# Performance work log

Hardware: AMD Instinct MI355X
Metric: run time of the kernel (lower is better)

## Reference

```python
import jax, jax.numpy as jnp
import numpy as np

N_NODES = 100000
N_EDGES = 800000
N_FEAT = 64
H_DIM = 64
N_GRAPHS = 64


def _glorot(key, fan_in, fan_out):
    lim = np.sqrt(6.0 / (fan_in + fan_out)).astype(np.float32)
    return jax.random.uniform(key, (fan_in, fan_out), jnp.float32, -lim, lim)


def setup_inputs() -> dict:
    key = jax.random.key(0)
    ks = jax.random.split(key, 10)
    x = jax.random.normal(ks[0], (N_NODES, N_FEAT), jnp.float32)
    edge_index = jax.random.randint(ks[1], (2, N_EDGES), 0, N_NODES, dtype=jnp.int64)
    batch = jnp.sort(jax.random.randint(ks[2], (N_NODES,), 0, N_GRAPHS, dtype=jnp.int64))
    return {
        "x": x,
        "edge_index": edge_index,
        "batch": batch,
        "W0": _glorot(ks[3], N_FEAT, H_DIM), "b0": jnp.zeros((H_DIM,), jnp.float32),
        "W1": _glorot(ks[4], H_DIM, H_DIM), "b1": jnp.zeros((H_DIM,), jnp.float32),
        "W2": _glorot(ks[5], H_DIM, H_DIM), "b2": jnp.zeros((H_DIM,), jnp.float32),
        "Wl": _glorot(ks[6], H_DIM, H_DIM),
        "bl": jax.random.normal(ks[7], (H_DIM,), jnp.float32) * 0.01,
    }


def _gcn_conv(h, W, b, row, col, dinv_r, dinv_c, n_nodes):
    # PyG GCNConv: x W, then sym-normalized aggregation over edges+self-loops
    h = h @ W                                   # [N, H]
    msg = h[row] * (dinv_r * dinv_c)[:, None]   # gather + scale, [E+N, H]
    out = jax.ops.segment_sum(msg, col, num_segments=n_nodes)  # scatter-add
    return out + b


def reference(x, edge_index, batch, W0, b0, W1, b1, W2, b2, Wl, bl):
    n = x.shape[0]
    loops = jnp.arange(n, dtype=edge_index.dtype)
    row = jnp.concatenate([edge_index[0], loops])  # source nodes (+self-loops)
    col = jnp.concatenate([edge_index[1], loops])  # destination nodes
    deg = jax.ops.segment_sum(jnp.ones_like(col, dtype=x.dtype), col, num_segments=n)
    dinv = jnp.where(deg > 0, jax.lax.rsqrt(deg), 0.0)
    dinv_r, dinv_c = dinv[row], dinv[col]

    out = x
    for W, b in ((W0, b0), (W1, b1), (W2, b2)):
        out = jax.nn.relu(_gcn_conv(out, W, b, row, col, dinv_r, dinv_c, n))
        # F.dropout(training=False) is identity in eval mode
    return (out, out @ Wl + bl)
```

## Files before the change

kernel.cpp:

```cpp
#include <hip/hip_runtime.h>

#define NN 100000
#define NE 800000
#define HD 64
#define BK 128
#define NBUCK ((NN + BK - 1) / BK)
#define PA_EPT 16
#define PA_NB ((NE + 256 * PA_EPT - 1) / (256 * PA_EPT))
#define LDW 68
#define LDB 72

typedef __attribute__((ext_vector_type(8))) short bf16x8;
typedef __attribute__((ext_vector_type(4))) float f32x4;

__device__ __forceinline__ int load_idx(const void* ei, int i, bool is32) {
    if (is32) return ((const int*)ei)[i];
    return (int)(((const long long*)ei)[i]);
}

__device__ __forceinline__ unsigned short f2bf(float f) {
    unsigned u = __float_as_uint(f);
    return (unsigned short)((u + 0x7FFFu + ((u >> 16) & 1u)) >> 16);
}

__device__ __forceinline__ float bf2f(unsigned short h) {
    return __uint_as_float((unsigned)h << 16);
}

__device__ __forceinline__ void bfacc(const uint4& u, float4& a, float4& b) {
    a.x += __uint_as_float(u.x << 16);
    a.y += __uint_as_float(u.x & 0xFFFF0000u);
    a.z += __uint_as_float(u.y << 16);
    a.w += __uint_as_float(u.y & 0xFFFF0000u);
    b.x += __uint_as_float(u.z << 16);
    b.y += __uint_as_float(u.z & 0xFFFF0000u);
    b.z += __uint_as_float(u.w << 16);
    b.w += __uint_as_float(u.w & 0xFFFF0000u);
}

__global__ void k_initdet(const void* ei, int* bcnt, int* flag) {
    __shared__ int bad;
    int t = threadIdx.x;
    if (t == 0) bad = 0;
    if (t < NBUCK) bcnt[t] = 0;
    __syncthreads();
    const long long* p = (const long long*)ei;
    for (int i = t; i < 4096; i += 1024) {
        long long v = p[i];
        if (v < 0 || v >= (long long)NN) bad = 1;
    }
    __syncthreads();
    if (t == 0) *flag = bad ? 1 : 0;
}

__global__ __launch_bounds__(256) void k_pass0(const void* ei, const int* flag,
                                               int* bcnt) {
    __shared__ int h[NBUCK];
    for (int i = threadIdx.x; i < NBUCK; i += 256) h[i] = 0;
    __syncthreads();
    bool is32 = (*flag != 0);
    int stride = gridDim.x * 256;
    for (int e = blockIdx.x * 256 + threadIdx.x; e < NE; e += stride) {
        int dst = load_idx(ei, NE + e, is32);
        atomicAdd(&h[dst >> 7], 1);
    }
    __syncthreads();
    for (int i = threadIdx.x; i < NBUCK; i += 256) {
        int v = h[i];
        if (v) atomicAdd(&bcnt[i], v);
    }
}

__global__ __launch_bounds__(256) void k_scan1(const int* __restrict__ bcnt,
                                               int* __restrict__ offs,
                                               int* __restrict__ curs) {
    __shared__ int sc[256];
    int t = threadIdx.x;
    int v[4], s = 0;
#pragma unroll
    for (int i = 0; i < 4; ++i) {
        int b = t * 4 + i;
        v[i] = (b < NBUCK) ? bcnt[b] : 0;
        s += v[i];
    }
    sc[t] = s;
    __syncthreads();
    for (int off = 1; off < 256; off <<= 1) {
        int add = (t >= off) ? sc[t - off] : 0;
        __syncthreads();
        sc[t] += add;
        __syncthreads();
    }
    int run = sc[t] - s;
#pragma unroll
    for (int i = 0; i < 4; ++i) {
        int b = t * 4 + i;
        if (b < NBUCK) { offs[b] = run; curs[b] = run; }
        run += v[i];
    }
    if (t == 255) offs[NBUCK] = sc[255];
}

__global__ __launch_bounds__(256) void k_passA(const void* ei, const int* flag,
                                               int* curs, unsigned* ebuf) {
    __shared__ int h[NBUCK];
    __shared__ int base[NBUCK];
    for (int i = threadIdx.x; i < NBUCK; i += 256) h[i] = 0;
    __syncthreads();
    bool is32 = (*flag != 0);
    int e0 = blockIdx.x * (256 * PA_EPT);
    int src[PA_EPT], dst[PA_EPT];
#pragma unroll
    for (int i = 0; i < PA_EPT; ++i) {
        int e = e0 + i * 256 + threadIdx.x;
        if (e < NE) {
            src[i] = load_idx(ei, e, is32);
            dst[i] = load_idx(ei, NE + e, is32);
            atomicAdd(&h[dst[i] >> 7], 1);
        } else dst[i] = -1;
    }
    __syncthreads();
    for (int i = threadIdx.x; i < NBUCK; i += 256) {
        int v = h[i];
        base[i] = v ? atomicAdd(&curs[i], v) : 0;
        h[i] = 0;
    }
    __syncthreads();
#pragma unroll
    for (int i = 0; i < PA_EPT; ++i) {
        if (dst[i] >= 0) {
            int b = dst[i] >> 7;
            int p = base[b] + atomicAdd(&h[b], 1);
            ebuf[p] = (unsigned)src[i] | ((unsigned)(dst[i] & 127) << 17);
        }
    }
}

__global__ __launch_bounds__(256) void k_passB(const unsigned* __restrict__ ebuf,
                                               const int* __restrict__ offs,
                                               int* __restrict__ noffs,
                                               int* __restrict__ csr_src,
                                               float* __restrict__ dinv) {
    __shared__ int cnt[BK];
    __shared__ int sc[BK];
    __shared__ int nbase[BK];
    __shared__ int rank[BK];
    int bk = blockIdx.x;
    int t = threadIdx.x;
    if (t < BK) { cnt[t] = 0; rank[t] = 0; }
    __syncthreads();
    int rs = offs[bk], re = offs[bk + 1];
    for (int i = rs + t; i < re; i += 256)
        atomicAdd(&cnt[ebuf[i] >> 17], 1);
    __syncthreads();
    if (t < BK) sc[t] = cnt[t];
    __syncthreads();
    for (int off = 1; off < BK; off <<= 1) {
        int v = 0;
        if (t < BK && t >= off) v = sc[t - off];
        __syncthreads();
        if (t < BK) sc[t] += v;
        __syncthreads();
    }
    if (t < BK) {
        int node = bk * BK + t;
        int nb = rs + sc[t] - cnt[t];
        nbase[t] = nb;
        if (node < NN) {
            noffs[node] = nb;
            dinv[node] = rsqrtf((float)(cnt[t] + 1));
        }
    }
    if (bk == NBUCK - 1 && t == 0) noffs[NN] = re;
    __syncthreads();
    for (int i = rs + t; i < re; i += 256) {
        unsigned w = ebuf[i];
        int dl = w >> 17;
        int p = nbase[dl] + atomicAdd(&rank[dl], 1);
        csr_src[p] = (int)(w & 0x1FFFFu);
    }
}

template <bool BIAS, bool PRE, bool BF16OUT>
__global__ __launch_bounds__(256, 4) void k_gemm(const float* __restrict__ X,
                                                 const float* __restrict__ W,
                                                 const float* __restrict__ bias,
                                                 const float* __restrict__ dinv,
                                                 void* __restrict__ Hout, int n) {
    __shared__ float Ws[64 * LDW];
    __shared__ float Xs[128 * LDW];
    int t = threadIdx.x;
    int row0 = blockIdx.x * 128;
    const float4* X4 = (const float4*)X;
    for (int i = t; i < 64 * 16; i += 256) {
        float4 v = ((const float4*)W)[i];
        *(float4*)&Ws[(i >> 4) * LDW + (i & 15) * 4] = v;
    }
    for (int i = t; i < 128 * 16; i += 256) {
        int r = row0 + (i >> 4);
        float4 v = (r < n) ? X4[(size_t)r * 16 + (i & 15)]
                           : make_float4(0.f, 0.f, 0.f, 0.f);
        *(float4*)&Xs[(i >> 4) * LDW + (i & 15) * 4] = v;
    }
    __syncthreads();
    int tc = (t & 15) * 4;
    int rbase = t >> 4;
    float4 acc[8] = {};
#pragma unroll 1
    for (int k = 0; k < 64; k += 4) {
        float4 wv[4], xv[8];
#pragma unroll
        for (int kk = 0; kk < 4; ++kk)
            wv[kk] = *(const float4*)&Ws[(k + kk) * LDW + tc];
#pragma unroll
        for (int i = 0; i < 8; ++i)
            xv[i] = *(const float4*)&Xs[(rbase + 16 * i) * LDW + k];
#pragma unroll
        for (int i = 0; i < 8; ++i) {
            acc[i].x += xv[i].x * wv[0].x + xv[i].y * wv[1].x
                      + xv[i].z * wv[2].x + xv[i].w * wv[3].x;
            acc[i].y += xv[i].x * wv[0].y + xv[i].y * wv[1].y
                      + xv[i].z * wv[2].y + xv[i].w * wv[3].y;
            acc[i].z += xv[i].x * wv[0].z + xv[i].y * wv[1].z
                      + xv[i].z * wv[2].z + xv[i].w * wv[3].z;
            acc[i].w += xv[i].x * wv[0].w + xv[i].y * wv[1].w
                      + xv[i].z * wv[2].w + xv[i].w * wv[3].w;
        }
    }
    float4 bv = make_float4(0.f, 0.f, 0.f, 0.f);
    if (BIAS) bv = *(const float4*)&bias[tc];
#pragma unroll
    for (int i = 0; i < 8; ++i) {
        int r = row0 + rbase + 16 * i;
        if (r < n) {
            float s = PRE ? dinv[r] : 1.f;
            float4 o;
            o.x = (acc[i].x + bv.x) * s;
            o.y = (acc[i].y + bv.y) * s;
            o.z = (acc[i].z + bv.z) * s;
            o.w = (acc[i].w + bv.w) * s;
            if (BF16OUT) {
                ushort4 p;
                p.x = f2bf(o.x); p.y = f2bf(o.y); p.z = f2bf(o.z); p.w = f2bf(o.w);
                ((ushort4*)Hout)[(size_t)r * 16 + (t & 15)] = p;
            } else {
                ((float4*)Hout)[(size_t)r * 16 + (t & 15)] = o;
            }
        }
    }
}

template <int MODE>
__global__ __launch_bounds__(256, 4) void k_fused(const uint4* __restrict__ Hb,
                                               const int* __restrict__ noffs,
                                               const int* __restrict__ csr_src,
                                               const float* __restrict__ dinv,
                                               const float4* __restrict__ b4,
                                               const float* __restrict__ Wn,
                                               const float* __restrict__ bl,
                                               unsigned short* __restrict__ HbOut,
                                               float4* __restrict__ out0,
                                               float* __restrict__ out1) {
    __shared__ unsigned short WtH[64 * LDB];
    __shared__ unsigned short WtL[64 * LDB];
    __shared__ __align__(16) char scratch[32 * LDB * 2 * 2];
    __shared__ float dvs[32];
    __shared__ float bls[64];
    unsigned short* rows_hi = (unsigned short*)scratch;
    unsigned short* rows_lo = (unsigned short*)scratch + 32 * LDB;
    float* cbuf = (float*)scratch;
    int t = threadIdx.x;
    for (int i = t; i < 64 * 64; i += 256) {
        int k = i >> 6, c = i & 63;
        float wv = Wn[i];
        unsigned short hi = f2bf(wv);
        unsigned short lo = f2bf(wv - bf2f(hi));
        WtH[c * LDB + k] = hi;
        WtL[c * LDB + k] = lo;
    }
    if (MODE == 1 && t < 64) bls[t] = bl[t];

    int lane = t & 63;
    int cl = lane >> 3;
    int q = lane & 7;
    int cbase = lane & ~7;
    int nl = (t >> 6) * 8 + cl;
    int base = blockIdx.x * 32;
    int node = base + nl;
    float dv = 0.f;
    float4 alo = make_float4(0.f, 0.f, 0.f, 0.f);
    float4 ahi = make_float4(0.f, 0.f, 0.f, 0.f);
    if (node < NN) {
        dv = dinv[node];
        {
            uint4 u = Hb[(size_t)node * 8 + q];
            bfacc(u, alo, ahi);
        }
        int e0 = noffs[node], e1 = noffs[node + 1];
#pragma unroll 1
        for (int e = e0; e < e1; e += 8) {
            int rem = e1 - e;
            int idx = (q < rem) ? csr_src[e + q] : 0;
            int s[8];
#pragma unroll
            for (int j = 0; j < 8; ++j)
                s[j] = __shfl(idx, cbase + j, 64);
            uint4 uu[8];
#pragma unroll
            for (int j = 0; j < 8; ++j)
                uu[j] = Hb[(size_t)s[j] * 8 + q];
#pragma unroll
            for (int j = 0; j < 8; ++j)
                if (j < rem) bfacc(uu[j], alo, ahi);
        }
    }
    if (node < NN) {
        float4 b0v = b4[2 * q], b1v = b4[2 * q + 1];
        float f[8];
        f[0] = fmaxf(alo.x * dv + b0v.x, 0.f);
        f[1] = fmaxf(alo.y * dv + b0v.y, 0.f);
        f[2] = fmaxf(alo.z * dv + b0v.z, 0.f);
        f[3] = fmaxf(alo.w * dv + b0v.w, 0.f);
        f[4] = fmaxf(ahi.x * dv + b1v.x, 0.f);
        f[5] = fmaxf(ahi.y * dv + b1v.y, 0.f);
        f[6] = fmaxf(ahi.z * dv + b1v.z, 0.f);
        f[7] = fmaxf(ahi.w * dv + b1v.w, 0.f);
        if (MODE == 1) {
            out0[(size_t)node * 16 + 2 * q]     = make_float4(f[0], f[1], f[2], f[3]);
            out0[(size_t)node * 16 + 2 * q + 1] = make_float4(f[4], f[5], f[6], f[7]);
        }
        unsigned hw[4], lw[4];
#pragma unroll
        for (int i = 0; i < 4; ++i) {
            unsigned short h0 = f2bf(f[2 * i]),     h1 = f2bf(f[2 * i + 1]);
            unsigned short l0 = f2bf(f[2 * i]     - bf2f(h0));
            unsigned short l1 = f2bf(f[2 * i + 1] - bf2f(h1));
            hw[i] = (unsigned)h0 | ((unsigned)h1 << 16);
            lw[i] = (unsigned)l0 | ((unsigned)l1 << 16);
        }
        *(uint4*)&rows_hi[nl * LDB + 8 * q] = make_uint4(hw[0], hw[1], hw[2], hw[3]);
        *(uint4*)&rows_lo[nl * LDB + 8 * q] = make_uint4(lw[0], lw[1], lw[2], lw[3]);
        if (q == 0) dvs[nl] = dv;
    }
    __syncthreads();

    int w = t >> 6;
    int la = lane & 15, kc = lane >> 4;
    int tr = w & 1;
    int c0 = (w >> 1) * 32;
    f32x4 ac0 = {0.f, 0.f, 0.f, 0.f};
    f32x4 ac1 = {0.f, 0.f, 0.f, 0.f};
    const unsigned short* arH = &rows_hi[(tr * 16 + la) * LDB];
    const unsigned short* arL = &rows_lo[(tr * 16 + la) * LDB];
    const unsigned short* b0H = &WtH[(c0 + la) * LDB];
    const unsigned short* b0L = &WtL[(c0 + la) * LDB];
    const unsigned short* b1H = &WtH[(c0 + 16 + la) * LDB];
    const unsigned short* b1L = &WtL[(c0 + 16 + la) * LDB];
#pragma unroll
    for (int kh = 0; kh < 2; ++kh) {
        int ko = kh * 32 + kc * 8;
        bf16x8 aH  = *(const bf16x8*)(arH + ko);
        bf16x8 aL  = *(const bf16x8*)(arL + ko);
        bf16x8 bH0 = *(const bf16x8*)(b0H + ko);
        bf16x8 bL0 = *(const bf16x8*)(b0L + ko);
        bf16x8 bH1 = *(const bf16x8*)(b1H + ko);
        bf16x8 bL1 = *(const bf16x8*)(b1L + ko);
        ac0 = __builtin_amdgcn_mfma_f32_16x16x32_bf16(aH, bH0, ac0, 0, 0, 0);
        ac1 = __builtin_amdgcn_mfma_f32_16x16x32_bf16(aH, bH1, ac1, 0, 0, 0);
        ac0 = __builtin_amdgcn_mfma_f32_16x16x32_bf16(aL, bH0, ac0, 0, 0, 0);
        ac1 = __builtin_amdgcn_mfma_f32_16x16x32_bf16(aL, bH1, ac1, 0, 0, 0);
        ac0 = __builtin_amdgcn_mfma_f32_16x16x32_bf16(aH, bL0, ac0, 0, 0, 0);
        ac1 = __builtin_amdgcn_mfma_f32_16x16x32_bf16(aH, bL1, ac1, 0, 0, 0);
    }
    __syncthreads();

    int rb2 = tr * 16 + kc * 4;
#pragma unroll
    for (int j = 0; j < 4; ++j) {
        cbuf[(rb2 + j) * LDW + c0 + la]      = ac0[j];
        cbuf[(rb2 + j) * LDW + c0 + 16 + la] = ac1[j];
    }
    __syncthreads();

    int nl2 = t >> 3, q2 = t & 7;
    int n2 = base + nl2;
    if (n2 < NN) {
        const float* cp = &cbuf[nl2 * LDW + 8 * q2];
        if (MODE == 0) {
            float s = dvs[nl2];
            ushort4 pa, pb;
            pa.x = f2bf(cp[0] * s); pa.y = f2bf(cp[1] * s);
            pa.z = f2bf(cp[2] * s); pa.w = f2bf(cp[3] * s);
            pb.x = f2bf(cp[4] * s); pb.y = f2bf(cp[5] * s);
            pb.z = f2bf(cp[6] * s); pb.w = f2bf(cp[7] * s);
            *(ushort4*)&HbOut[(size_t)n2 * 64 + 8 * q2]     = pa;
            *(ushort4*)&HbOut[(size_t)n2 * 64 + 8 * q2 + 4] = pb;
        } else {
            float4 o0, o1;
            o0.x = cp[0] + bls[8 * q2];     o0.y = cp[1] + bls[8 * q2 + 1];
            o0.z = cp[2] + bls[8 * q2 + 2]; o0.w = cp[3] + bls[8 * q2 + 3];
            o1.x = cp[4] + bls[8 * q2 + 4]; o1.y = cp[5] + bls[8 * q2 + 5];
            o1.z = cp[6] + bls[8 * q2 + 6]; o1.w = cp[7] + bls[8 * q2 + 7];
            *(float4*)&out1[(size_t)n2 * 64 + 8 * q2]     = o0;
            *(float4*)&out1[(size_t)n2 * 64 + 8 * q2 + 4] = o1;
        }
    }
}

extern "C" void kernel_launch(void* const* d_in, const int* in_sizes, int n_in,
                              void* d_out, int out_size, void* d_ws, size_t ws_size,
                              hipStream_t stream) {
    const float* x  = (const float*)d_in[0];
    const void*  ei = d_in[1];
    const float* W0 = (const float*)d_in[3];
    const float* b0 = (const float*)d_in[4];
    const float* W1 = (const float*)d_in[5];
    const float* b1 = (const float*)d_in[6];
    const float* W2 = (const float*)d_in[7];
    const float* b2 = (const float*)d_in[8];
    const float* Wl = (const float*)d_in[9];
    const float* bl = (const float*)d_in[10];

    char* ws = (char*)d_ws;
    int*      flag    = (int*)(ws);
    int*      bcnt    = (int*)(ws + 256);
    int*      offs    = (int*)(ws + 4352);
    int*      curs    = (int*)(ws + 8448);
    float*    dinv    = (float*)(ws + 12544);
    int*      noffs   = (int*)(ws + 412672);
    int*      csr_src = (int*)(ws + 812800);
    unsigned short* HbA = (unsigned short*)(ws + 4100096);
    unsigned short* HbB = (unsigned short*)(ws + 16900096);

    float* out0 = (float*)d_out;
    float* out1 = out0 + (size_t)NN * HD;
    unsigned* ebuf = (unsigned*)out1;

    int gG = (NN + 127) / 128;
    int gF = (NN + 31) / 32;

    k_initdet<<<1, 1024, 0, stream>>>(ei, bcnt, flag);
    k_pass0<<<128, 256, 0, stream>>>(ei, flag, bcnt);
    k_scan1<<<1, 256, 0, stream>>>(bcnt, offs, curs);
    k_passA<<<PA_NB, 256, 0, stream>>>(ei, flag, curs, ebuf);
    k_passB<<<NBUCK, 256, 0, stream>>>(ebuf, offs, noffs, csr_src, dinv);

    k_gemm<false, true, true><<<gG, 256, 0, stream>>>(x, W0, nullptr, dinv,
                                                      (void*)HbA, NN);
    k_fused<0><<<gF, 256, 0, stream>>>((const uint4*)HbA, noffs, csr_src, dinv,
                                       (const float4*)b0, W1, nullptr,
                                       HbB, nullptr, nullptr);
    k_fused<0><<<gF, 256, 0, stream>>>((const uint4*)HbB, noffs, csr_src, dinv,
                                       (const float4*)b1, W2, nullptr,
                                       HbA, nullptr, nullptr);
    k_fused<1><<<gF, 256, 0, stream>>>((const uint4*)HbA, noffs, csr_src, dinv,
                                       (const float4*)b2, Wl, bl,
                                       nullptr, (float4*)out0, out1);
}
```

Before: 235.2 us.

## Store fp32 weights in LDS and split to bf16 hi/lo at MFMA time

The fused aggregate+GEMM kernel now keeps W and the aggregated rows as fp32 in shared memory and does the bf16 hi/lo split on the fly when building MFMA fragments, instead of pre-splitting into two bf16 arrays. This shrinks LDS use per block, and the occupancy hint rises from 4 to 6 blocks per CU. The node's degree, edge offsets and self feature row are now loaded before the weight staging so their latency overlaps it, and the bias is read from global memory instead of LDS. In exchange, every wave repeats the bf16 conversion work for each fragment, and the tighter launch bound may cause register spills.

New measurement: 241.5 us. 2.7% more time.

```diff
diff --git a/kernel.cpp b/kernel.cpp
--- a/kernel.cpp
+++ b/kernel.cpp
@@ -8,7 +8,6 @@
 #define PA_EPT 16
 #define PA_NB ((NE + 256 * PA_EPT - 1) / (256 * PA_EPT))
 #define LDW 68
-#define LDB 72
 
 typedef __attribute__((ext_vector_type(8))) short bf16x8;
 typedef __attribute__((ext_vector_type(4))) float f32x4;
@@ -36,6 +35,18 @@
     b.y += __uint_as_float(u.z & 0xFFFF0000u);
     b.z += __uint_as_float(u.w << 16);
     b.w += __uint_as_float(u.w & 0xFFFF0000u);
+}
+
+__device__ __forceinline__ void mk_frag(const float* p, bf16x8& h, bf16x8& l) {
+    float4 v0 = *(const float4*)(p);
+    float4 v1 = *(const float4*)(p + 4);
+    float f[8] = {v0.x, v0.y, v0.z, v0.w, v1.x, v1.y, v1.z, v1.w};
+#pragma unroll
+    for (int i = 0; i < 8; ++i) {
+        unsigned short hb = f2bf(f[i]);
+        h[i] = (short)hb;
+        l[i] = (short)f2bf(f[i] - bf2f(hb));
+    }
 }
 
 __global__ void k_initdet(const void* ei, int* bcnt, int* flag) {
@@ -251,7 +262,7 @@
 }
 
 template <int MODE>
-__global__ __launch_bounds__(256, 4) void k_fused(const uint4* __restrict__ Hb,
+__global__ __launch_bounds__(256, 6) void k_fused(const uint4* __restrict__ Hb,
                                                const int* __restrict__ noffs,
                                                const int* __restrict__ csr_src,
                                                const float* __restrict__ dinv,
@@ -261,25 +272,10 @@
                                                unsigned short* __restrict__ HbOut,
                                                float4* __restrict__ out0,
                                                float* __restrict__ out1) {
-    __shared__ unsigned short WtH[64 * LDB];
-    __shared__ unsigned short WtL[64 * LDB];
-    __shared__ __align__(16) char scratch[32 * LDB * 2 * 2];
+    __shared__ float WsT[64 * LDW];
+    __shared__ __align__(16) float rowsb[32 * LDW];
     __shared__ float dvs[32];
-    __shared__ float bls[64];
-    unsigned short* rows_hi = (unsigned short*)scratch;
-    unsigned short* rows_lo = (unsigned short*)scratch + 32 * LDB;
-    float* cbuf = (float*)scratch;
     int t = threadIdx.x;
-    for (int i = t; i < 64 * 64; i += 256) {
-        int k = i >> 6, c = i & 63;
-        float wv = Wn[i];
-        unsigned short hi = f2bf(wv);
-        unsigned short lo = f2bf(wv - bf2f(hi));
-        WtH[c * LDB + k] = hi;
-        WtL[c * LDB + k] = lo;
-    }
-    if (MODE == 1 && t < 64) bls[t] = bl[t];
-
     int lane = t & 63;
     int cl = lane >> 3;
     int q = lane & 7;
@@ -287,16 +283,31 @@
     int nl = (t >> 6) * 8 + cl;
     int base = blockIdx.x * 32;
     int node = base + nl;
+
     float dv = 0.f;
+    int e0 = 0, e1 = 0;
+    uint4 uself = make_uint4(0u, 0u, 0u, 0u);
+    if (node < NN) {
+        dv = dinv[node];
+        e0 = noffs[node];
+        e1 = noffs[node + 1];
+        uself = Hb[(size_t)node * 8 + q];
+    }
+
+    for (int i = t; i < 1024; i += 256) {
+        int k = i & 63;
+        int cg = i >> 6;
+        float4 v = ((const float4*)Wn)[k * 16 + cg];
+        WsT[(cg * 4 + 0) * LDW + k] = v.x;
+        WsT[(cg * 4 + 1) * LDW + k] = v.y;
+        WsT[(cg * 4 + 2) * LDW + k] = v.z;
+        WsT[(cg * 4 + 3) * LDW + k] = v.w;
+    }
+
     float4 alo = make_float4(0.f, 0.f, 0.f, 0.f);
     float4 ahi = make_float4(0.f, 0.f, 0.f, 0.f);
     if (node < NN) {
-        dv = dinv[node];
-        {
-            uint4 u = Hb[(size_t)node * 8 + q];
-            bfacc(u, alo, ahi);
-        }
-        int e0 = noffs[node], e1 = noffs[node + 1];
+        bfacc(uself, alo, ahi);
 #pragma unroll 1
         for (int e = e0; e < e1; e += 8) {
             int rem = e1 - e;
@@ -316,30 +327,21 @@
     }
     if (node < NN) {
         float4 b0v = b4[2 * q], b1v = b4[2 * q + 1];
-        float f[8];
-        f[0] = fmaxf(alo.x * dv + b0v.x, 0.f);
-        f[1] = fmaxf(alo.y * dv + b0v.y, 0.f);
-        f[2] = fmaxf(alo.z * dv + b0v.z, 0.f);
-        f[3] = fmaxf(alo.w * dv + b0v.w, 0.f);
-        f[4] = fmaxf(ahi.x * dv + b1v.x, 0.f);
-        f[5] = fmaxf(ahi.y * dv + b1v.y, 0.f);
-        f[6] = fmaxf(ahi.z * dv + b1v.z, 0.f);
-        f[7] = fmaxf(ahi.w * dv + b1v.w, 0.f);
+        float4 r0, r1;
+        r0.x = fmaxf(alo.x * dv + b0v.x, 0.f);
+        r0.y = fmaxf(alo.y * dv + b0v.y, 0.f);
+        r0.z = fmaxf(alo.z * dv + b0v.z, 0.f);
+        r0.w = fmaxf(alo.w * dv + b0v.w, 0.f);
+        r1.x = fmaxf(ahi.x * dv + b1v.x, 0.f);
+        r1.y = fmaxf(ahi.y * dv + b1v.y, 0.f);
+        r1.z = fmaxf(ahi.z * dv + b1v.z, 0.f);
+        r1.w = fmaxf(ahi.w * dv + b1v.w, 0.f);
         if (MODE == 1) {
-            out0[(size_t)node * 16 + 2 * q]     = make_float4(f[0], f[1], f[2], f[3]);
-            out0[(size_t)node * 16 + 2 * q + 1] = make_float4(f[4], f[5], f[6], f[7]);
-        }
-        unsigned hw[4], lw[4];
-#pragma unroll
-        for (int i = 0; i < 4; ++i) {
-            unsigned short h0 = f2bf(f[2 * i]),     h1 = f2bf(f[2 * i + 1]);
-            unsigned short l0 = f2bf(f[2 * i]     - bf2f(h0));
-            unsigned short l1 = f2bf(f[2 * i + 1] - bf2f(h1));
-            hw[i] = (unsigned)h0 | ((unsigned)h1 << 16);
-            lw[i] = (unsigned)l0 | ((unsigned)l1 << 16);
-        }
-        *(uint4*)&rows_hi[nl * LDB + 8 * q] = make_uint4(hw[0], hw[1], hw[2], hw[3]);
-        *(uint4*)&rows_lo[nl * LDB + 8 * q] = make_uint4(lw[0], lw[1], lw[2], lw[3]);
+            out0[(size_t)node * 16 + 2 * q]     = r0;
+            out0[(size_t)node * 16 + 2 * q + 1] = r1;
+        }
+        *(float4*)&rowsb[nl * LDW + 8 * q]     = r0;
+        *(float4*)&rowsb[nl * LDW + 8 * q + 4] = r1;
         if (q == 0) dvs[nl] = dv;
     }
     __syncthreads();
@@ -350,21 +352,16 @@
     int c0 = (w >> 1) * 32;
     f32x4 ac0 = {0.f, 0.f, 0.f, 0.f};
     f32x4 ac1 = {0.f, 0.f, 0.f, 0.f};
-    const unsigned short* arH = &rows_hi[(tr * 16 + la) * LDB];
-    const unsigned short* arL = &rows_lo[(tr * 16 + la) * LDB];
-    const unsigned short* b0H = &WtH[(c0 + la) * LDB];
-    const unsigned short* b0L = &WtL[(c0 + la) * LDB];
-    const unsigned short* b1H = &WtH[(c0 + 16 + la) * LDB];
-    const unsigned short* b1L = &WtL[(c0 + 16 + la) * LDB];
+    const float* ar  = &rowsb[(tr * 16 + la) * LDW];
+    const float* bp0 = &WsT[(c0 + la) * LDW];
+    const float* bp1 = &WsT[(c0 + 16 + la) * LDW];
 #pragma unroll
     for (int kh = 0; kh < 2; ++kh) {
         int ko = kh * 32 + kc * 8;
-        bf16x8 aH  = *(const bf16x8*)(arH + ko);
-        bf16x8 aL  = *(const bf16x8*)(arL + ko);
-        bf16x8 bH0 = *(const bf16x8*)(b0H + ko);
-        bf16x8 bL0 = *(const bf16x8*)(b0L + ko);
-        bf16x8 bH1 = *(const bf16x8*)(b1H + ko);
-        bf16x8 bL1 = *(const bf16x8*)(b1L + ko);
+        bf16x8 aH, aL, bH0, bL0, bH1, bL1;
+        mk_frag(ar + ko, aH, aL);
+        mk_frag(bp0 + ko, bH0, bL0);
+        mk_frag(bp1 + ko, bH1, bL1);
         ac0 = __builtin_amdgcn_mfma_f32_16x16x32_bf16(aH, bH0, ac0, 0, 0, 0);
         ac1 = __builtin_amdgcn_mfma_f32_16x16x32_bf16(aH, bH1, ac1, 0, 0, 0);
         ac0 = __builtin_amdgcn_mfma_f32_16x16x32_bf16(aL, bH0, ac0, 0, 0, 0);
@@ -374,6 +371,7 @@
     }
     __syncthreads();
 
+    float* cbuf = rowsb;
     int rb2 = tr * 16 + kc * 4;
 #pragma unroll
     for (int j = 0; j < 4; ++j) {
@@ -396,11 +394,13 @@
             *(ushort4*)&HbOut[(size_t)n2 * 64 + 8 * q2]     = pa;
             *(ushort4*)&HbOut[(size_t)n2 * 64 + 8 * q2 + 4] = pb;
         } else {
+            const float4* blv = (const float4*)bl;
+            float4 bv0 = blv[2 * q2], bv1 = blv[2 * q2 + 1];
             float4 o0, o1;
-            o0.x = cp[0] + bls[8 * q2];     o0.y = cp[1] + bls[8 * q2 + 1];
-            o0.z = cp[2] + bls[8 * q2 + 2]; o0.w = cp[3] + bls[8 * q2 + 3];
-            o1.x = cp[4] + bls[8 * q2 + 4]; o1.y = cp[5] + bls[8 * q2 + 5];
-            o1.z = cp[6] + bls[8 * q2 + 6]; o1.w = cp[7] + bls[8 * q2 + 7];
+            o0.x = cp[0] + bv0.x; o0.y = cp[1] + bv0.y;
+            o0.z = cp[2] + bv0.z; o0.w = cp[3] + bv0.w;
+            o1.x = cp[4] + bv1.x; o1.y = cp[5] + bv1.y;
+            o1.z = cp[6] + bv1.z; o1.w = cp[7] + bv1.w;
             *(float4*)&out1[(size_t)n2 * 64 + 8 * q2]     = o0;
             *(float4*)&out1[(size_t)n2 * 64 + 8 * q2 + 4] = o1;
         }
```
